# Kernel tuning notes

Measured on AMD Instinct MI355X. Metric: run time of the kernel, lower is better.

## Reference

```python
import jax, jax.numpy as jnp
import numpy as np

B, T, D, H, QK = 4, 2048, 1024, 16, 64
MAX_WAVELENGTH = 10000


def apply_rope(x, positions):
    # x: [B, T, H, d]; positions: [B, T] int
    d = x.shape[-1]
    fraction = 2 * jnp.arange(0, d // 2, dtype=jnp.int32) / d
    timescale = MAX_WAVELENGTH ** fraction  # [d/2]
    sinusoid = positions[..., None] / timescale[None, :]  # [B, T, d/2]
    sinusoid = sinusoid[..., None, :]  # [B, T, 1, d/2]
    sin, cos = jnp.sin(sinusoid), jnp.cos(sinusoid)
    x1, x2 = jnp.split(x, 2, axis=-1)
    return jnp.concatenate([x1 * cos - x2 * sin, x2 * cos + x1 * sin], axis=-1).astype(x.dtype)


def rms_norm(x, scale):
    var = jnp.mean(jnp.square(x), axis=-1, keepdims=True)
    return x * jax.lax.rsqrt(var + 1e-6) * (1 + scale)


def setup_inputs() -> dict:
    key = jax.random.key(0)
    ks = jax.random.split(key, 12)
    s = 0.02
    pos = jnp.broadcast_to(jnp.arange(T, dtype=jnp.int32), (B, T))
    causal = jnp.tril(jnp.ones((T, T), dtype=bool))[None, None]  # [1,1,T,T]
    return {
        "q": jax.random.normal(ks[0], (B, T, D), jnp.float32),
        "kv": jax.random.normal(ks[1], (B, T, D), jnp.float32),
        "mask": jnp.broadcast_to(causal, (B, 1, T, T)),
        "q_positions": pos,
        "kv_positions": pos,
        "Wq": jax.random.normal(ks[2], (D, H * QK), jnp.float32) * s,
        "bq": jnp.zeros((H * QK,), jnp.float32),
        "Wk": jax.random.normal(ks[3], (D, H * QK), jnp.float32) * s,
        "bk": jnp.zeros((H * QK,), jnp.float32),
        "Wv": jax.random.normal(ks[4], (D, H * QK), jnp.float32) * s,
        "bv": jnp.zeros((H * QK,), jnp.float32),
        "q_scale": jnp.zeros((QK,), jnp.float32),
        "k_scale": jnp.zeros((QK,), jnp.float32),
        "head_scale": jnp.zeros((1, H, 1), jnp.float32),
        "Wo": jax.random.normal(ks[5], (H * QK, D), jnp.float32) * s,
        "bo": jnp.zeros((D,), jnp.float32),
    }


def reference(q, kv, mask, q_positions, kv_positions, Wq, bq, Wk, bk, Wv, bv,
              q_scale, k_scale, head_scale, Wo, bo):
    qh = (q @ Wq + bq).reshape(B, T, H, QK)
    kh = (kv @ Wk + bk).reshape(B, T, H, QK)
    vh = (kv @ Wv + bv).reshape(B, T, H, QK)
    # qk layer norm (RMSNorm with (1+scale))
    qh = rms_norm(qh, q_scale)
    kh = rms_norm(kh, k_scale)
    # RoPE
    qh = apply_rope(qh, q_positions)
    kh = apply_rope(kh, kv_positions)
    # attention
    logits = jnp.einsum('bthd,bThd->bhtT', qh, kh) / np.sqrt(QK).astype(q.dtype)
    logits = jnp.where(mask, logits, jnp.finfo(logits.dtype).min)
    weights = jax.nn.softmax(logits, axis=-1)
    weights = jnp.where(mask, weights, 0)
    attn = jnp.einsum('bhtT,bThd->bthd', weights, vh)
    attn = attn * (1 + head_scale)  # [1,H,1] broadcasts over (t,h,d)
    return attn.reshape(B, T, H * QK) @ Wo + bo
```

## Files before the change

### kernel.cpp

```cpp
#include <hip/hip_runtime.h>
#include <math.h>

#define BB 4
#define TT 2048
#define DD 1024
#define HH 16
#define QKD 64
#define MM (BB*TT)
#define NN 1024
#define KK 1024

#define BKG 64
#define NTSG (KK/BKG)

typedef unsigned short u16;
typedef __attribute__((ext_vector_type(8))) short short8;
typedef __attribute__((ext_vector_type(4))) float float4v;

__device__ __forceinline__ u16 f2bf(float f) {
    union { float f; unsigned u; } v; v.f = f;
    unsigned r = (v.u + 0x7FFFu + ((v.u >> 16) & 1u)) >> 16;
    return (u16)r;
}

__device__ __forceinline__ unsigned cvt_pk_bf16(float lo, float hi) {
    unsigned r;
    asm("v_cvt_pk_bf16_f32 %0, %1, %2" : "=v"(r) : "v"(lo), "v"(hi));
    return r;
}

typedef __attribute__((address_space(3))) unsigned lds_u32_t;
typedef __attribute__((address_space(1))) const unsigned glb_u32_t;
__device__ __forceinline__ void gl2lds16(const u16* g, u16* l) {
    __builtin_amdgcn_global_load_lds((glb_u32_t*)g, (lds_u32_t*)l, 16, 0, 0);
}

__device__ __forceinline__ int swz_slot(int row, int slot) {
    return slot ^ (row & 7);
}

__global__ __launch_bounds__(256) void acast_kernel(
    const float* __restrict__ a, const float* __restrict__ b,
    u16* __restrict__ da, u16* __restrict__ db)
{
    const float* s = blockIdx.y ? b : a;
    u16* d = blockIdx.y ? db : da;
    size_t i = ((size_t)blockIdx.x * 256 + threadIdx.x) * 4;
    float4 v = *(const float4*)&s[i];
    ushort4 o = { f2bf(v.x), f2bf(v.y), f2bf(v.z), f2bf(v.w) };
    *(ushort4*)&d[i] = o;
}

__global__ __launch_bounds__(256) void wt_kernel(
    const float* __restrict__ Wq, const float* __restrict__ Wk,
    const float* __restrict__ Wv, const float* __restrict__ Wo,
    u16* __restrict__ dstbase)
{
    const int z = blockIdx.z;
    const float* src = (z == 0) ? Wq : (z == 1) ? Wk : (z == 2) ? Wv : Wo;
    u16* out = dstbase + (size_t)z * (KK * NN);
    const int bi = blockIdx.y, bj = blockIdx.x;
    __shared__ float tile[64][65];
    const int t = threadIdx.x;
    #pragma unroll
    for (int p = 0; p < 4; p++) {
        int idx = p * 256 + t;
        int r = idx >> 4, c4 = (idx & 15) << 2;
        float4 v = *(const float4*)&src[(size_t)(bi * 64 + r) * NN + bj * 64 + c4];
        tile[r][c4 + 0] = v.x; tile[r][c4 + 1] = v.y;
        tile[r][c4 + 2] = v.z; tile[r][c4 + 3] = v.w;
    }
    __syncthreads();
    #pragma unroll
    for (int p = 0; p < 4; p++) {
        int idx = p * 256 + t;
        int rn = idx >> 4, c4 = (idx & 15) << 2;
        ushort4 o = { f2bf(tile[c4 + 0][rn]), f2bf(tile[c4 + 1][rn]),
                      f2bf(tile[c4 + 2][rn]), f2bf(tile[c4 + 3][rn]) };
        *(ushort4*)&out[(size_t)(bj * 64 + rn) * KK + bi * 64 + c4] = o;
    }
}

__device__ __forceinline__ void gemm256_mainloop(
    const u16* __restrict__ A, const u16* __restrict__ Bt,
    int m0, int n0, u16* __restrict__ sh, float4v (&acc)[8][4])
{
    const int tid = threadIdx.x;
    const int lane = tid & 63;
    const int l15 = lane & 15, lg = lane >> 4;
    const int wave = tid >> 6;
    const int wm = wave >> 2, wn = wave & 3;

    const u16* gA[4]; const u16* gB[4]; int ld_off[4];
    #pragma unroll
    for (int i = 0; i < 4; i++) {
        const int c = tid + i * 512;
        const int r = c >> 3, sp = c & 7;
        const int gs = swz_slot(r, sp);
        gA[i] = A  + (size_t)(m0 + r) * KK + gs * 8;
        gB[i] = Bt + (size_t)(n0 + r) * KK + gs * 8;
        ld_off[i] = c * 8;
    }

    auto issue = [&](int buf, int k0) {
        u16* dA = sh + buf * 32768;
        u16* dB = dA + 16384;
        #pragma unroll
        for (int i = 0; i < 4; i++) gl2lds16(gA[i] + k0, dA + ld_off[i]);
        #pragma unroll
        for (int i = 0; i < 4; i++) gl2lds16(gB[i] + k0, dB + ld_off[i]);
    };

    issue(0, 0);

    for (int t = 0; t < NTSG; t++) {
        const int buf = t & 1;
        if (t + 1 < NTSG) {
            issue(buf ^ 1, (t + 1) * BKG);
            asm volatile("s_waitcnt vmcnt(8)" ::: "memory");
        } else {
            asm volatile("s_waitcnt vmcnt(0)" ::: "memory");
        }
        __builtin_amdgcn_s_barrier();
        __builtin_amdgcn_sched_barrier(0);

        const u16* cA = sh + buf * 32768;
        const u16* cB = cA + 16384;

        #pragma unroll
        for (int kk = 0; kk < 2; kk++) {
            short8 af[8], bf[4];
            #pragma unroll
            for (int x = 0; x < 8; x++) {
                const int ra = wm * 128 + x * 16 + l15;
                af[x] = *(const short8*)(cA + ra * 64 + swz_slot(ra, kk * 4 + lg) * 8);
            }
            #pragma unroll
            for (int x = 0; x < 4; x++) {
                const int rb = wn * 64 + x * 16 + l15;
                bf[x] = *(const short8*)(cB + rb * 64 + swz_slot(rb, kk * 4 + lg) * 8);
            }
            __builtin_amdgcn_s_setprio(1);
            #pragma unroll
            for (int mi = 0; mi < 8; mi++)
                #pragma unroll
                for (int nj = 0; nj < 4; nj++)
                    acc[mi][nj] = __builtin_amdgcn_mfma_f32_16x16x32_bf16(af[mi], bf[nj], acc[mi][nj], 0, 0, 0);
            __builtin_amdgcn_s_setprio(0);
        }

        __builtin_amdgcn_s_barrier();
        __builtin_amdgcn_sched_barrier(0);
    }
}

__device__ __forceinline__ void xcd_swizzle_4x32(int& m_idx, int& n_idx) {
    const int flat = blockIdx.y * 4 + blockIdx.x;
    const int xcd = flat & 7, q = flat >> 3;
    m_idx = xcd * 4 + (q & 3);
    n_idx = q >> 2;
}

__global__ __launch_bounds__(512, 2) void qkv_gemm(
    const u16* __restrict__ qb, const u16* __restrict__ kvb,
    const u16* __restrict__ Wt,
    const float* __restrict__ bq, const float* __restrict__ bk, const float* __restrict__ bv,
    const int* __restrict__ qpos, const int* __restrict__ kpos,
    const float* __restrict__ q_scale, const float* __restrict__ k_scale,
    u16* __restrict__ qh, u16* __restrict__ kh, u16* __restrict__ vt)
{
    __shared__ __align__(16) u16 sh[65536];

    const int z = blockIdx.z;
    const u16* A        = (z == 0) ? qb : kvb;
    const u16* B        = Wt + (size_t)z * (KK * NN);
    const float* bias   = (z == 0) ? bq : (z == 1) ? bk : bv;
    const float* scl    = (z == 0) ? q_scale : k_scale;
    const int* pos_arr  = (z == 0) ? qpos : kpos;
    u16* dst            = (z == 0) ? qh : (z == 1) ? kh : vt;

    int m_idx, n_idx;
    xcd_swizzle_4x32(m_idx, n_idx);
    const int m0 = m_idx * 256, n0 = n_idx * 256;

    float4v acc[8][4];
    #pragma unroll
    for (int i = 0; i < 8; i++)
        #pragma unroll
        for (int j = 0; j < 4; j++) acc[i][j] = (float4v){0.f, 0.f, 0.f, 0.f};

    gemm256_mainloop(A, B, m0, n0, sh, acc);

    const int tid = threadIdx.x;
    const int lane = tid & 63, wave = tid >> 6;
    const int l15 = lane & 15, lg = lane >> 4;
    const int wm = wave >> 2, wn = wave & 3;

    float bia[4], sc[4];
    #pragma unroll
    for (int nj = 0; nj < 4; nj++) {
        bia[nj] = bias[n0 + wn * 64 + nj * 16 + l15];
        sc[nj]  = 1.0f + scl[nj * 16 + l15];
    }
    float invts[2];
    #pragma unroll
    for (int p = 0; p < 2; p++)
        invts[p] = powf(10000.0f, -(float)(p * 16 + l15) * (1.0f / 32.0f));

    const float QMUL = 0.125f * 1.44269504088896340736f;
    const int bb_ = m0 >> 11;
    const int t0g = m0 & 2047;

    if (z < 2) {
        #pragma unroll
        for (int p = 0; p < 2; p++) {
            __syncthreads();
            if (wm == p) {
                #pragma unroll
                for (int mi = 0; mi < 8; mi++) {
                    #pragma unroll
                    for (int r = 0; r < 4; r++) {
                        const int tl = mi * 16 + lg * 4 + r;
                        const int m = m0 + p * 128 + tl;
                        const int b = m >> 11, t = m & 2047;
                        float v[4];
                        #pragma unroll
                        for (int nj = 0; nj < 4; nj++) v[nj] = acc[mi][nj][r] + bia[nj];

                        float ss = v[0]*v[0] + v[1]*v[1] + v[2]*v[2] + v[3]*v[3];
                        ss += __shfl_xor(ss, 1);
                        ss += __shfl_xor(ss, 2);
                        ss += __shfl_xor(ss, 4);
                        ss += __shfl_xor(ss, 8);
                        float rn = rsqrtf(ss * (1.0f / 64.0f) + 1e-6f);
                        #pragma unroll
                        for (int nj = 0; nj < 4; nj++) v[nj] = v[nj] * rn * sc[nj];

                        const float pos = (float)pos_arr[b * TT + t];
                        #pragma unroll
                        for (int pp = 0; pp < 2; pp++) {
                            float ang = pos * invts[pp];
                            float s = sinf(ang), c = cosf(ang);
                            float x1 = v[pp], x2 = v[pp + 2];
                            v[pp]     = x1 * c - x2 * s;
                            v[pp + 2] = x2 * c + x1 * s;
                        }
                        if (z == 0) {
                            #pragma unroll
                            for (int nj = 0; nj < 4; nj++) v[nj] *= QMUL;
                        }
                        #pragma unroll
                        for (int nj = 0; nj < 4; nj++) {
                            const int dl = wn * 64 + nj * 16 + l15;
                            sh[tl * 256 + (dl ^ ((tl & 7) << 3))] = f2bf(v[nj]);
                        }
                    }
                }
            }
            __syncthreads();
            #pragma unroll
            for (int it = 0; it < 8; it++) {
                int idx = it * 512 + tid;
                int tl  = idx >> 5;
                int c8  = (idx & 31) << 3;
                short8 v8 = *(const short8*)&sh[tl * 256 + (c8 ^ ((tl & 7) << 3))];
                int cg = n0 + c8;
                int hh_ = cg >> 6, dih = cg & 63;
                int t = t0g + p * 128 + tl;
                *(short8*)&dst[((size_t)(bb_ * HH + hh_) * TT + t) * QKD + dih] = v8;
            }
        }
    } else {
        #pragma unroll
        for (int p = 0; p < 2; p++) {
            __syncthreads();
            if (wm == p) {
                #pragma unroll
                for (int mi = 0; mi < 8; mi++) {
                    #pragma unroll
                    for (int r = 0; r < 4; r++) {
                        const int tl = mi * 16 + lg * 4 + r;
                        #pragma unroll
                        for (int nj = 0; nj < 4; nj++) {
                            const int dl = wn * 64 + nj * 16 + l15;
                            sh[dl * 128 + (tl ^ ((dl & 7) << 3))] = f2bf(acc[mi][nj][r] + bia[nj]);
                        }
                    }
                }
            }
            __syncthreads();
            #pragma unroll
            for (int it = 0; it < 8; it++) {
                int idx = it * 512 + tid;
                int dl  = idx >> 4;
                int tc  = (idx & 15) << 3;
                short8 v8 = *(const short8*)&sh[dl * 128 + (tc ^ ((dl & 7) << 3))];
                int dg = n0 + dl;
                int hh_ = dg >> 6, dih = dg & 63;
                *(short8*)&vt[((size_t)(bb_ * HH + hh_) * QKD + dih) * TT + t0g + p * 128 + tc] = v8;
            }
        }
    }
}

__global__ __launch_bounds__(512, 2) void out_gemm(
    const u16* __restrict__ A, const u16* __restrict__ Bt,
    const float* __restrict__ bo, float* __restrict__ out)
{
    __shared__ __align__(16) u16 sh[65536];

    int m_idx, n_idx;
    xcd_swizzle_4x32(m_idx, n_idx);
    const int m0 = m_idx * 256, n0 = n_idx * 256;

    float4v acc[8][4];
    #pragma unroll
    for (int i = 0; i < 8; i++)
        #pragma unroll
        for (int j = 0; j < 4; j++) acc[i][j] = (float4v){0.f, 0.f, 0.f, 0.f};

    gemm256_mainloop(A, Bt, m0, n0, sh, acc);

    const int lane = threadIdx.x & 63, wave = threadIdx.x >> 6;
    const int l15 = lane & 15, lg = lane >> 4;
    const int wm = wave >> 2, wn = wave & 3;

    float bov[4];
    #pragma unroll
    for (int nj = 0; nj < 4; nj++) bov[nj] = bo[n0 + wn * 64 + nj * 16 + l15];

    #pragma unroll
    for (int mi = 0; mi < 8; mi++)
        #pragma unroll
        for (int r = 0; r < 4; r++) {
            const int m = m0 + wm * 128 + mi * 16 + lg * 4 + r;
            float* op = out + (size_t)m * NN + n0 + wn * 64 + l15;
            #pragma unroll
            for (int nj = 0; nj < 4; nj++)
                op[nj * 16] = acc[mi][nj][r] + bov[nj];
        }
}

__global__ __launch_bounds__(256) void attn_mfma(
    const u16* __restrict__ qh, const u16* __restrict__ kh,
    const u16* __restrict__ vt, const float* __restrict__ head_scale,
    u16* __restrict__ out)
{
    __shared__ __align__(16) u16 Ks[2][64 * 64];
    __shared__ __align__(16) u16 Vs[2][64 * 64];
    __shared__ __align__(16) u16 Ps[4][16 * 64];

    const int b = blockIdx.z, h = blockIdx.y;
    const int qta = blockIdx.x;
    const int qtb = 31 - qta;
    const int t0a = qta * 64, t0b = qtb * 64;

    const int tid  = threadIdx.x;
    const int wave = tid >> 6, lane = tid & 63;
    const int l15 = lane & 15, lg = lane >> 4;
    const int l7 = l15 & 7;

    const size_t bh = (size_t)(b * HH + h);
    const u16* qbh  = qh + bh * TT * QKD;
    const u16* kbh  = kh + bh * TT * QKD;
    const u16* vtbh = vt + bh * QKD * TT;

    short8 qfA[2], qfB[2];
    #pragma unroll
    for (int kc = 0; kc < 2; kc++) {
        qfA[kc] = *(const short8*)(qbh + (size_t)(t0a + wave * 16 + l15) * QKD
                                    + kc * 32 + lg * 8);
        qfB[kc] = *(const short8*)(qbh + (size_t)(t0b + wave * 16 + l15) * QKD
                                    + kc * 32 + lg * 8);
    }

    auto stage = [&](int buf, int j0s) {
        #pragma unroll
        for (int rr = 0; rr < 2; rr++) {
            const int c   = rr * 256 + tid;
            const int row = c >> 3;
            const int g   = (c & 7) ^ (row & 7);
            u16* ldsK = &Ks[buf][(rr * 256 + (wave << 6)) * 8];
            u16* ldsV = &Vs[buf][(rr * 256 + (wave << 6)) * 8];
            gl2lds16(kbh  + (size_t)(j0s + row) * QKD + g * 8, ldsK);
            gl2lds16(vtbh + (size_t)row * TT + j0s + g * 8, ldsV);
        }
    };

    float4v oA[4], oB[4];
    #pragma unroll
    for (int nt = 0; nt < 4; nt++) {
        oA[nt] = (float4v){0.f, 0.f, 0.f, 0.f};
        oB[nt] = (float4v){0.f, 0.f, 0.f, 0.f};
    }
    float mA[4] = {-INFINITY, -INFINITY, -INFINITY, -INFINITY};
    float mB[4] = {-INFINITY, -INFINITY, -INFINITY, -INFINITY};
    float lA[4] = {0.f, 0.f, 0.f, 0.f};
    float lB[4] = {0.f, 0.f, 0.f, 0.f};

    auto flash_step = [&](int cur, int jt, int qt_self,
                          short8 (&qf)[2], float4v (&oa)[4],
                          float (&mr)[4], float (&lr)[4]) {
        float4v sarr[4];
        #pragma unroll
        for (int nt = 0; nt < 4; nt++) {
            float4v s = (float4v){0.f, 0.f, 0.f, 0.f};
            #pragma unroll
            for (int kc = 0; kc < 2; kc++) {
                const short8 bfrag = *(const short8*)
                    &Ks[cur][(nt * 16 + l15) * 64 + ((kc * 4 + lg) ^ l7) * 8];
                s = __builtin_amdgcn_mfma_f32_16x16x32_bf16(qf[kc], bfrag, s, 0, 0, 0);
            }
            sarr[nt] = s;
        }

        if (jt == qt_self) {
            const int qbase = qt_self * 64 + wave * 16 + lg * 4;
            #pragma unroll
            for (int nt = 0; nt < 4; nt++) {
                int jkey = jt * 64 + nt * 16 + l15;
                #pragma unroll
                for (int r = 0; r < 4; r++)
                    if (jkey > qbase + r) sarr[nt][r] = -INFINITY;
            }
        }

        float pm[4];
        #pragma unroll
        for (int r = 0; r < 4; r++) {
            float m = fmaxf(fmaxf(sarr[0][r], sarr[1][r]), fmaxf(sarr[2][r], sarr[3][r]));
            m = fmaxf(m, __shfl_xor(m, 1));
            m = fmaxf(m, __shfl_xor(m, 2));
            m = fmaxf(m, __shfl_xor(m, 4));
            m = fmaxf(m, __shfl_xor(m, 8));
            pm[r] = m;
        }
        float grow = fmaxf(fmaxf(pm[0] - mr[0], pm[1] - mr[1]),
                           fmaxf(pm[2] - mr[2], pm[3] - mr[3]));
        if (__any(grow > 8.0f)) {
            #pragma unroll
            for (int r = 0; r < 4; r++) {
                float mn = fmaxf(mr[r], pm[r]);
                float a  = exp2f(mr[r] - mn);
                mr[r] = mn;
                lr[r] *= a;
                #pragma unroll
                for (int nt = 0; nt < 4; nt++) oa[nt][r] *= a;
            }
        }

        u16* pw = Ps[wave];
        float lp[4] = {0.f, 0.f, 0.f, 0.f};
        #pragma unroll
        for (int nt = 0; nt < 4; nt++) {
            float p0 = exp2f(sarr[nt][0] - mr[0]);
            float p1 = exp2f(sarr[nt][1] - mr[1]);
            float p2 = exp2f(sarr[nt][2] - mr[2]);
            float p3 = exp2f(sarr[nt][3] - mr[3]);
            lp[0] += p0; lp[1] += p1; lp[2] += p2; lp[3] += p3;
            unsigned wlo = cvt_pk_bf16(p0, p1);
            unsigned whi = cvt_pk_bf16(p2, p3);
            const int gb = nt * 2 + (l15 >> 3);
            const int r0 = lg * 4;
            pw[(r0 + 0) * 64 + ((gb ^ ((r0 + 0) & 7))) * 8 + l7] = (u16)wlo;
            pw[(r0 + 1) * 64 + ((gb ^ ((r0 + 1) & 7))) * 8 + l7] = (u16)(wlo >> 16);
            pw[(r0 + 2) * 64 + ((gb ^ ((r0 + 2) & 7))) * 8 + l7] = (u16)whi;
            pw[(r0 + 3) * 64 + ((gb ^ ((r0 + 3) & 7))) * 8 + l7] = (u16)(whi >> 16);
        }
        #pragma unroll
        for (int r = 0; r < 4; r++) lr[r] += lp[r];

        short8 pf[2];
        #pragma unroll
        for (int kc = 0; kc < 2; kc++)
            pf[kc] = *(const short8*)&pw[l15 * 64 + ((kc * 4 + lg) ^ l7) * 8];

        #pragma unroll
        for (int nt = 0; nt < 4; nt++) {
            #pragma unroll
            for (int kc = 0; kc < 2; kc++) {
                const short8 vfrag = *(const short8*)
                    &Vs[cur][(nt * 16 + l15) * 64 + ((kc * 4 + lg) ^ l7) * 8];
                oa[nt] = __builtin_amdgcn_mfma_f32_16x16x32_bf16(pf[kc], vfrag, oa[nt], 0, 0, 0);
            }
        }
    };

    stage(0, 0);
    __syncthreads();

    const int njt = qtb + 1;
    for (int jt = 0; jt < njt; jt++) {
        const int cur = jt & 1;
        if (jt + 1 < njt) stage(cur ^ 1, (jt + 1) * 64);

        flash_step(cur, jt, qtb, qfB, oB, mB, lB);
        if (jt <= qta)
            flash_step(cur, jt, qta, qfA, oA, mA, lA);

        __syncthreads();
    }

    const float hs = 1.0f + head_scale[h];
    auto epilogue = [&](int t0, float4v (&oa)[4], float (&lr)[4]) {
        #pragma unroll
        for (int r = 0; r < 4; r++) {
            float l = lr[r];
            l += __shfl_xor(l, 1);
            l += __shfl_xor(l, 2);
            l += __shfl_xor(l, 4);
            l += __shfl_xor(l, 8);
            const int q = t0 + wave * 16 + lg * 4 + r;
            const float f = hs / l;
            u16* op = out + ((size_t)(b * TT + q) * NN) + h * QKD + l15;
            #pragma unroll
            for (int nt = 0; nt < 4; nt++)
                op[nt * 16] = f2bf(oa[nt][r] * f);
        }
    };
    epilogue(t0b, oB, lB);
    epilogue(t0a, oA, lA);
}

extern "C" void kernel_launch(void* const* d_in, const int* in_sizes, int n_in,
                              void* d_out, int out_size, void* d_ws, size_t ws_size,
                              hipStream_t stream)
{
    const float* q          = (const float*)d_in[0];
    const float* kv         = (const float*)d_in[1];
    const int*   qpos       = (const int*)d_in[3];
    const int*   kpos       = (const int*)d_in[4];
    const float* Wq         = (const float*)d_in[5];
    const float* bq         = (const float*)d_in[6];
    const float* Wk         = (const float*)d_in[7];
    const float* bk         = (const float*)d_in[8];
    const float* Wv         = (const float*)d_in[9];
    const float* bv         = (const float*)d_in[10];
    const float* q_scale    = (const float*)d_in[11];
    const float* k_scale    = (const float*)d_in[12];
    const float* head_scale = (const float*)d_in[13];
    const float* Wo         = (const float*)d_in[14];
    const float* bo         = (const float*)d_in[15];
    float* out = (float*)d_out;

    char* ws = (char*)d_ws;
    u16* qb     = (u16*)(ws);
    u16* kvb    = (u16*)(ws + (16u << 20));
    u16* Wt     = (u16*)(ws + (32u << 20));
    u16* qh_b   = (u16*)(ws + (40u << 20));
    u16* kh_b   = (u16*)(ws + (56u << 20));
    u16* vt_b   = (u16*)(ws + (72u << 20));
    u16* attn_b = (u16*)(ws + (88u << 20));

    acast_kernel<<<dim3(MM * DD / (256 * 4), 2), 256, 0, stream>>>(q, kv, qb, kvb);
    wt_kernel<<<dim3(16, 16, 4), 256, 0, stream>>>(Wq, Wk, Wv, Wo, Wt);
    qkv_gemm<<<dim3(NN / 256, MM / 256, 3), 512, 0, stream>>>(
        qb, kvb, Wt, bq, bk, bv, qpos, kpos, q_scale, k_scale, qh_b, kh_b, vt_b);
    attn_mfma<<<dim3(TT / 128, HH, BB), 256, 0, stream>>>(qh_b, kh_b, vt_b, head_scale, attn_b);
    out_gemm<<<dim3(NN / 256, MM / 256), 512, 0, stream>>>(attn_b, Wt + (size_t)3 * KK * NN, bo, out);
}
```

Measured before the change: 474.2 us.

## Switch projection GEMMs to 256x64 tiles with 4-wave blocks

Changes the QKV and output GEMMs from 256x256 tiles with 512 threads to 256x64 tiles with 256 threads. Each block now covers exactly one head, which simplifies the RMSNorm/RoPE epilogue and drops the two-pass staging through shared memory. LDS use per block shrinks and the grid grows fourfold, which helps occupancy and load balance. In exchange each block reuses its A tile across fewer columns, so more global/L2 traffic is spent re-reading A.

```diff
diff --git a/kernel.cpp b/kernel.cpp
--- a/kernel.cpp
+++ b/kernel.cpp
@@ -12,6 +12,7 @@
 
 #define BKG 64
 #define NTSG (KK/BKG)
+#define LDSBUF 20480
 
 typedef unsigned short u16;
 typedef __attribute__((ext_vector_type(8))) short short8;
@@ -81,34 +82,39 @@
     }
 }
 
-__device__ __forceinline__ void gemm256_mainloop(
+__device__ __forceinline__ void gemm_mainloop_256x64(
     const u16* __restrict__ A, const u16* __restrict__ Bt,
-    int m0, int n0, u16* __restrict__ sh, float4v (&acc)[8][4])
+    int m0, int n0, u16* __restrict__ sh, float4v (&acc)[4][4])
 {
     const int tid = threadIdx.x;
     const int lane = tid & 63;
     const int l15 = lane & 15, lg = lane >> 4;
     const int wave = tid >> 6;
-    const int wm = wave >> 2, wn = wave & 3;
-
-    const u16* gA[4]; const u16* gB[4]; int ld_off[4];
-    #pragma unroll
-    for (int i = 0; i < 4; i++) {
-        const int c = tid + i * 512;
+
+    const u16* gA[8]; int offA[8];
+    #pragma unroll
+    for (int i = 0; i < 8; i++) {
+        const int c = tid + i * 256;
         const int r = c >> 3, sp = c & 7;
-        const int gs = swz_slot(r, sp);
-        gA[i] = A  + (size_t)(m0 + r) * KK + gs * 8;
-        gB[i] = Bt + (size_t)(n0 + r) * KK + gs * 8;
-        ld_off[i] = c * 8;
+        gA[i] = A + (size_t)(m0 + r) * KK + swz_slot(r, sp) * 8;
+        offA[i] = c * 8;
+    }
+    const u16* gB[2]; int offB[2];
+    #pragma unroll
+    for (int i = 0; i < 2; i++) {
+        const int c = tid + i * 256;
+        const int r = c >> 3, sp = c & 7;
+        gB[i] = Bt + (size_t)(n0 + r) * KK + swz_slot(r, sp) * 8;
+        offB[i] = c * 8;
     }
 
     auto issue = [&](int buf, int k0) {
-        u16* dA = sh + buf * 32768;
+        u16* dA = sh + buf * LDSBUF;
         u16* dB = dA + 16384;
         #pragma unroll
-        for (int i = 0; i < 4; i++) gl2lds16(gA[i] + k0, dA + ld_off[i]);
-        #pragma unroll
-        for (int i = 0; i < 4; i++) gl2lds16(gB[i] + k0, dB + ld_off[i]);
+        for (int i = 0; i < 8; i++) gl2lds16(gA[i] + k0, dA + offA[i]);
+        #pragma unroll
+        for (int i = 0; i < 2; i++) gl2lds16(gB[i] + k0, dB + offB[i]);
     };
 
     issue(0, 0);
@@ -117,32 +123,32 @@
         const int buf = t & 1;
         if (t + 1 < NTSG) {
             issue(buf ^ 1, (t + 1) * BKG);
-            asm volatile("s_waitcnt vmcnt(8)" ::: "memory");
+            asm volatile("s_waitcnt vmcnt(10)" ::: "memory");
         } else {
             asm volatile("s_waitcnt vmcnt(0)" ::: "memory");
         }
         __builtin_amdgcn_s_barrier();
         __builtin_amdgcn_sched_barrier(0);
 
-        const u16* cA = sh + buf * 32768;
+        const u16* cA = sh + buf * LDSBUF;
         const u16* cB = cA + 16384;
 
         #pragma unroll
         for (int kk = 0; kk < 2; kk++) {
-            short8 af[8], bf[4];
-            #pragma unroll
-            for (int x = 0; x < 8; x++) {
-                const int ra = wm * 128 + x * 16 + l15;
+            short8 af[4], bf[4];
+            #pragma unroll
+            for (int x = 0; x < 4; x++) {
+                const int ra = wave * 64 + x * 16 + l15;
                 af[x] = *(const short8*)(cA + ra * 64 + swz_slot(ra, kk * 4 + lg) * 8);
             }
             #pragma unroll
             for (int x = 0; x < 4; x++) {
-                const int rb = wn * 64 + x * 16 + l15;
+                const int rb = x * 16 + l15;
                 bf[x] = *(const short8*)(cB + rb * 64 + swz_slot(rb, kk * 4 + lg) * 8);
             }
             __builtin_amdgcn_s_setprio(1);
             #pragma unroll
-            for (int mi = 0; mi < 8; mi++)
+            for (int mi = 0; mi < 4; mi++)
                 #pragma unroll
                 for (int nj = 0; nj < 4; nj++)
                     acc[mi][nj] = __builtin_amdgcn_mfma_f32_16x16x32_bf16(af[mi], bf[nj], acc[mi][nj], 0, 0, 0);
@@ -154,14 +160,14 @@
     }
 }
 
-__device__ __forceinline__ void xcd_swizzle_4x32(int& m_idx, int& n_idx) {
-    const int flat = blockIdx.y * 4 + blockIdx.x;
+__device__ __forceinline__ void xcd_swizzle_16x32(int& m_idx, int& n_idx) {
+    const int flat = blockIdx.y * 16 + blockIdx.x;
     const int xcd = flat & 7, q = flat >> 3;
     m_idx = xcd * 4 + (q & 3);
     n_idx = q >> 2;
 }
 
-__global__ __launch_bounds__(512, 2) void qkv_gemm(
+__global__ __launch_bounds__(256, 2) void qkv_gemm(
     const u16* __restrict__ qb, const u16* __restrict__ kvb,
     const u16* __restrict__ Wt,
     const float* __restrict__ bq, const float* __restrict__ bk, const float* __restrict__ bv,
@@ -169,7 +175,7 @@
     const float* __restrict__ q_scale, const float* __restrict__ k_scale,
     u16* __restrict__ qh, u16* __restrict__ kh, u16* __restrict__ vt)
 {
-    __shared__ __align__(16) u16 sh[65536];
+    __shared__ __align__(16) u16 sh[2 * LDSBUF];
 
     const int z = blockIdx.z;
     const u16* A        = (z == 0) ? qb : kvb;
@@ -180,26 +186,26 @@
     u16* dst            = (z == 0) ? qh : (z == 1) ? kh : vt;
 
     int m_idx, n_idx;
-    xcd_swizzle_4x32(m_idx, n_idx);
-    const int m0 = m_idx * 256, n0 = n_idx * 256;
-
-    float4v acc[8][4];
-    #pragma unroll
-    for (int i = 0; i < 8; i++)
+    xcd_swizzle_16x32(m_idx, n_idx);
+    const int m0 = m_idx * 256, n0 = n_idx * 64;
+    const int h = n_idx;
+
+    float4v acc[4][4];
+    #pragma unroll
+    for (int i = 0; i < 4; i++)
         #pragma unroll
         for (int j = 0; j < 4; j++) acc[i][j] = (float4v){0.f, 0.f, 0.f, 0.f};
 
-    gemm256_mainloop(A, B, m0, n0, sh, acc);
+    gemm_mainloop_256x64(A, B, m0, n0, sh, acc);
 
     const int tid = threadIdx.x;
     const int lane = tid & 63, wave = tid >> 6;
     const int l15 = lane & 15, lg = lane >> 4;
-    const int wm = wave >> 2, wn = wave & 3;
 
     float bia[4], sc[4];
     #pragma unroll
     for (int nj = 0; nj < 4; nj++) {
-        bia[nj] = bias[n0 + wn * 64 + nj * 16 + l15];
+        bia[nj] = bias[n0 + nj * 16 + l15];
         sc[nj]  = 1.0f + scl[nj * 16 + l15];
     }
     float invts[2];
@@ -211,130 +217,112 @@
     const int bb_ = m0 >> 11;
     const int t0g = m0 & 2047;
 
+    __syncthreads();
+
     if (z < 2) {
         #pragma unroll
-        for (int p = 0; p < 2; p++) {
-            __syncthreads();
-            if (wm == p) {
-                #pragma unroll
-                for (int mi = 0; mi < 8; mi++) {
+        for (int mi = 0; mi < 4; mi++) {
+            #pragma unroll
+            for (int r = 0; r < 4; r++) {
+                const int tl = wave * 64 + mi * 16 + lg * 4 + r;
+                const int m = m0 + tl;
+                const int b = m >> 11, t = m & 2047;
+                float v[4];
+                #pragma unroll
+                for (int nj = 0; nj < 4; nj++) v[nj] = acc[mi][nj][r] + bia[nj];
+
+                float ss = v[0]*v[0] + v[1]*v[1] + v[2]*v[2] + v[3]*v[3];
+                ss += __shfl_xor(ss, 1);
+                ss += __shfl_xor(ss, 2);
+                ss += __shfl_xor(ss, 4);
+                ss += __shfl_xor(ss, 8);
+                float rn = rsqrtf(ss * (1.0f / 64.0f) + 1e-6f);
+                #pragma unroll
+                for (int nj = 0; nj < 4; nj++) v[nj] = v[nj] * rn * sc[nj];
+
+                const float pos = (float)pos_arr[b * TT + t];
+                #pragma unroll
+                for (int pp = 0; pp < 2; pp++) {
+                    float ang = pos * invts[pp];
+                    float s = sinf(ang), c = cosf(ang);
+                    float x1 = v[pp], x2 = v[pp + 2];
+                    v[pp]     = x1 * c - x2 * s;
+                    v[pp + 2] = x2 * c + x1 * s;
+                }
+                if (z == 0) {
                     #pragma unroll
-                    for (int r = 0; r < 4; r++) {
-                        const int tl = mi * 16 + lg * 4 + r;
-                        const int m = m0 + p * 128 + tl;
-                        const int b = m >> 11, t = m & 2047;
-                        float v[4];
-                        #pragma unroll
-                        for (int nj = 0; nj < 4; nj++) v[nj] = acc[mi][nj][r] + bia[nj];
-
-                        float ss = v[0]*v[0] + v[1]*v[1] + v[2]*v[2] + v[3]*v[3];
-                        ss += __shfl_xor(ss, 1);
-                        ss += __shfl_xor(ss, 2);
-                        ss += __shfl_xor(ss, 4);
-                        ss += __shfl_xor(ss, 8);
-                        float rn = rsqrtf(ss * (1.0f / 64.0f) + 1e-6f);
-                        #pragma unroll
-                        for (int nj = 0; nj < 4; nj++) v[nj] = v[nj] * rn * sc[nj];
-
-                        const float pos = (float)pos_arr[b * TT + t];
-                        #pragma unroll
-                        for (int pp = 0; pp < 2; pp++) {
-                            float ang = pos * invts[pp];
-                            float s = sinf(ang), c = cosf(ang);
-                            float x1 = v[pp], x2 = v[pp + 2];
-                            v[pp]     = x1 * c - x2 * s;
-                            v[pp + 2] = x2 * c + x1 * s;
-                        }
-                        if (z == 0) {
-                            #pragma unroll
-                            for (int nj = 0; nj < 4; nj++) v[nj] *= QMUL;
-                        }
-                        #pragma unroll
-                        for (int nj = 0; nj < 4; nj++) {
-                            const int dl = wn * 64 + nj * 16 + l15;
-                            sh[tl * 256 + (dl ^ ((tl & 7) << 3))] = f2bf(v[nj]);
-                        }
-                    }
+                    for (int nj = 0; nj < 4; nj++) v[nj] *= QMUL;
                 }
-            }
-            __syncthreads();
-            #pragma unroll
-            for (int it = 0; it < 8; it++) {
-                int idx = it * 512 + tid;
-                int tl  = idx >> 5;
-                int c8  = (idx & 31) << 3;
-                short8 v8 = *(const short8*)&sh[tl * 256 + (c8 ^ ((tl & 7) << 3))];
-                int cg = n0 + c8;
-                int hh_ = cg >> 6, dih = cg & 63;
-                int t = t0g + p * 128 + tl;
-                *(short8*)&dst[((size_t)(bb_ * HH + hh_) * TT + t) * QKD + dih] = v8;
-            }
+                #pragma unroll
+                for (int nj = 0; nj < 4; nj++)
+                    sh[tl * 64 + nj * 16 + l15] = f2bf(v[nj]);
+            }
+        }
+        __syncthreads();
+        #pragma unroll
+        for (int it = 0; it < 8; it++) {
+            int idx = it * 256 + tid;
+            int tl  = idx >> 3;
+            int c8  = (idx & 7) << 3;
+            short8 v8 = *(const short8*)&sh[tl * 64 + c8];
+            *(short8*)&dst[((size_t)(bb_ * HH + h) * TT + t0g + tl) * QKD + c8] = v8;
         }
     } else {
         #pragma unroll
-        for (int p = 0; p < 2; p++) {
-            __syncthreads();
-            if (wm == p) {
-                #pragma unroll
-                for (int mi = 0; mi < 8; mi++) {
-                    #pragma unroll
-                    for (int r = 0; r < 4; r++) {
-                        const int tl = mi * 16 + lg * 4 + r;
-                        #pragma unroll
-                        for (int nj = 0; nj < 4; nj++) {
-                            const int dl = wn * 64 + nj * 16 + l15;
-                            sh[dl * 128 + (tl ^ ((dl & 7) << 3))] = f2bf(acc[mi][nj][r] + bia[nj]);
-                        }
-                    }
+        for (int mi = 0; mi < 4; mi++) {
+            #pragma unroll
+            for (int r = 0; r < 4; r++) {
+                const int tl = wave * 64 + mi * 16 + lg * 4 + r;
+                #pragma unroll
+                for (int nj = 0; nj < 4; nj++) {
+                    const int dl = nj * 16 + l15;
+                    sh[dl * 256 + (tl ^ ((dl & 7) << 3))] = f2bf(acc[mi][nj][r] + bia[nj]);
                 }
             }
-            __syncthreads();
-            #pragma unroll
-            for (int it = 0; it < 8; it++) {
-                int idx = it * 512 + tid;
-                int dl  = idx >> 4;
-                int tc  = (idx & 15) << 3;
-                short8 v8 = *(const short8*)&sh[dl * 128 + (tc ^ ((dl & 7) << 3))];
-                int dg = n0 + dl;
-                int hh_ = dg >> 6, dih = dg & 63;
-                *(short8*)&vt[((size_t)(bb_ * HH + hh_) * QKD + dih) * TT + t0g + p * 128 + tc] = v8;
-            }
-        }
-    }
-}
-
-__global__ __launch_bounds__(512, 2) void out_gemm(
+        }
+        __syncthreads();
+        #pragma unroll
+        for (int it = 0; it < 8; it++) {
+            int idx = it * 256 + tid;
+            int dl  = idx >> 5;
+            int tc  = (idx & 31) << 3;
+            short8 v8 = *(const short8*)&sh[dl * 256 + (tc ^ ((dl & 7) << 3))];
+            *(short8*)&vt[((size_t)(bb_ * HH + h) * QKD + dl) * TT + t0g + tc] = v8;
+        }
+    }
+}
+
+__global__ __launch_bounds__(256, 2) void out_gemm(
     const u16* __restrict__ A, const u16* __restrict__ Bt,
     const float* __restrict__ bo, float* __restrict__ out)
 {
-    __shared__ __align__(16) u16 sh[65536];
+    __shared__ __align__(16) u16 sh[2 * LDSBUF];
 
     int m_idx, n_idx;
-    xcd_swizzle_4x32(m_idx, n_idx);
-    const int m0 = m_idx * 256, n0 = n_idx * 256;
-
-    float4v acc[8][4];
-    #pragma unroll
-    for (int i = 0; i < 8; i++)
+    xcd_swizzle_16x32(m_idx, n_idx);
+    const int m0 = m_idx * 256, n0 = n_idx * 64;
+
+    float4v acc[4][4];
+    #pragma unroll
+    for (int i = 0; i < 4; i++)
         #pragma unroll
         for (int j = 0; j < 4; j++) acc[i][j] = (float4v){0.f, 0.f, 0.f, 0.f};
 
-    gemm256_mainloop(A, Bt, m0, n0, sh, acc);
+    gemm_mainloop_256x64(A, Bt, m0, n0, sh, acc);
 
     const int lane = threadIdx.x & 63, wave = threadIdx.x >> 6;
     const int l15 = lane & 15, lg = lane >> 4;
-    const int wm = wave >> 2, wn = wave & 3;
 
     float bov[4];
     #pragma unroll
-    for (int nj = 0; nj < 4; nj++) bov[nj] = bo[n0 + wn * 64 + nj * 16 + l15];
-
-    #pragma unroll
-    for (int mi = 0; mi < 8; mi++)
+    for (int nj = 0; nj < 4; nj++) bov[nj] = bo[n0 + nj * 16 + l15];
+
+    #pragma unroll
+    for (int mi = 0; mi < 4; mi++)
         #pragma unroll
         for (int r = 0; r < 4; r++) {
-            const int m = m0 + wm * 128 + mi * 16 + lg * 4 + r;
-            float* op = out + (size_t)m * NN + n0 + wn * 64 + l15;
+            const int m = m0 + wave * 64 + mi * 16 + lg * 4 + r;
+            float* op = out + (size_t)m * NN + n0 + l15;
             #pragma unroll
             for (int nj = 0; nj < 4; nj++)
                 op[nj * 16] = acc[mi][nj][r] + bov[nj];
@@ -554,8 +542,8 @@
 
     acast_kernel<<<dim3(MM * DD / (256 * 4), 2), 256, 0, stream>>>(q, kv, qb, kvb);
     wt_kernel<<<dim3(16, 16, 4), 256, 0, stream>>>(Wq, Wk, Wv, Wo, Wt);
-    qkv_gemm<<<dim3(NN / 256, MM / 256, 3), 512, 0, stream>>>(
+    qkv_gemm<<<dim3(NN / 64, MM / 256, 3), 256, 0, stream>>>(
         qb, kvb, Wt, bq, bk, bv, qpos, kpos, q_scale, k_scale, qh_b, kh_b, vt_b);
     attn_mfma<<<dim3(TT / 128, HH, BB), 256, 0, stream>>>(qh_b, kh_b, vt_b, head_scale, attn_b);
-    out_gemm<<<dim3(NN / 256, MM / 256), 512, 0, stream>>>(attn_b, Wt + (size_t)3 * KK * NN, bo, out);
-}
+    out_gemm<<<dim3(NN / 64, MM / 256), 256, 0, stream>>>(attn_b, Wt + (size_t)3 * KK * NN, bo, out);
+}
```

New measurement: 428.0 us. 1.11x faster.
